# Kernel optimization log

Measured on AMD Instinct MI355X. Metric: run time of the kernel, lower is better.

The kernel has to match this reference:

```python
import jax, jax.numpy as jnp
import numpy as np

BETA_THRESH = 0.1   # threshold fraction in forward
BETA_IPOT = 0.5     # IPOT entropic beta
ITERATION = 30


def setup_inputs() -> dict:
    key = jax.random.key(0)
    k1, k2 = jax.random.split(key)
    bs, n, m, d = 64, 512, 512, 768
    return {
        "local_features_1": jax.random.normal(k1, (bs, n, d), dtype=jnp.float32),
        "local_features_2": jax.random.normal(k2, (bs, m, d), dtype=jnp.float32),
    }


def _wasserstein_loss(x, y):
    # x: (bs, n, d), y: (bs, m, d)
    # cost_matrix_batch_torch normalizes over the feature dim (dim=1 of bs*d*n layout)
    xn = x / (jnp.linalg.norm(x, axis=2, keepdims=True) + 1e-12)
    yn = y / (jnp.linalg.norm(y, axis=2, keepdims=True) + 1e-12)
    # cost_matrix returns (1 - cos).transpose(2,1); forward transposes back -> (bs, n, m)
    cos_distance = 1.0 - jnp.einsum("bnd,bmd->bnm", xn, yn)
    # global min/max threshold + relu
    min_score = cos_distance.min()
    max_score = cos_distance.max()
    threshold = min_score + BETA_THRESH * (max_score - min_score)
    C = jax.nn.relu(cos_distance - threshold)  # (bs, n, m)
    bs, n, m = C.shape
    A = jnp.exp(-C / BETA_IPOT)
    T0 = jnp.ones((bs, n, m), dtype=C.dtype)
    sigma0 = jnp.full((bs, m, 1), 1.0 / m, dtype=C.dtype)

    def step(carry, _):
        T, sigma = carry
        Q = A * T                                      # (bs, n, m)
        delta = 1.0 / (n * jnp.matmul(Q, sigma))       # (bs, n, 1)
        a = jnp.matmul(jnp.swapaxes(Q, 1, 2), delta)   # (bs, m, 1)
        sigma = 1.0 / (m * a)                          # (bs, m, 1)
        T = delta * Q * jnp.swapaxes(sigma, 1, 2)      # (bs, n, m)
        return (T, sigma), None

    (T, _), _ = jax.lax.scan(step, (T0, sigma0), None, length=ITERATION)
    # batch_trace(C^T @ T) == sum_ij C_ij * T_ij per batch element
    distance = jnp.einsum("bnm,bnm->b", C, T)
    # IPOT_distance returns -distance; loss is its mean
    return (-distance).mean()


def reference(local_features_1, local_features_2):
    return _wasserstein_loss(local_features_1, local_features_2)
```

## Files before the change

### kernel.cpp

```cpp
#include <hip/hip_runtime.h>
#include <hip/hip_fp16.h>

#define NN 512
#define DD 768

typedef _Float16 half8 __attribute__((ext_vector_type(8)));
typedef _Float16 half4 __attribute__((ext_vector_type(4)));
typedef _Float16 half2v __attribute__((ext_vector_type(2)));
typedef float f32x4 __attribute__((ext_vector_type(4)));

__device__ __forceinline__ int f2ord(float f) {
  int i = __float_as_int(f);
  return i < 0 ? (i ^ 0x7fffffff) : i;
}
__device__ __forceinline__ float ord2f(int i) {
  return __int_as_float(i < 0 ? (i ^ 0x7fffffff) : i);
}

__device__ __forceinline__ void glds16(const void* g, void* l) {
  __builtin_amdgcn_global_load_lds((const __attribute__((address_space(1))) void*)g,
                                   (__attribute__((address_space(3))) void*)l, 16, 0, 0);
}

__global__ __launch_bounds__(256) void k_norm(const float* __restrict__ f1,
                                              const float* __restrict__ f2,
                                              __half* __restrict__ xn,
                                              __half* __restrict__ yn,
                                              int* __restrict__ cnt) {
  if (blockIdx.x == 0) {
    int t = threadIdx.x;
    if (t < 64) { cnt[t * 16] = 0; cnt[1024 + t * 16] = 0; }
    if (t == 0) cnt[2048] = 0;
  }
  int row = blockIdx.x * 4 + (threadIdx.x >> 6);
  int lane = threadIdx.x & 63;
  int r = row & 32767;
  const float* src = (row < 32768 ? f1 : f2) + (size_t)r * DD;
  __half* dst = (row < 32768 ? xn : yn) + (size_t)r * DD;
  f32x4 v0 = *(const f32x4*)(src + lane * 4);
  f32x4 v1 = *(const f32x4*)(src + lane * 4 + 256);
  f32x4 v2 = *(const f32x4*)(src + lane * 4 + 512);
  float s = v0[0]*v0[0] + v0[1]*v0[1] + v0[2]*v0[2] + v0[3]*v0[3]
          + v1[0]*v1[0] + v1[1]*v1[1] + v1[2]*v1[2] + v1[3]*v1[3]
          + v2[0]*v2[0] + v2[1]*v2[1] + v2[2]*v2[2] + v2[3]*v2[3];
  #pragma unroll
  for (int m = 1; m < 64; m <<= 1) s += __shfl_xor(s, m, 64);
  float f = 1.0f / (sqrtf(s) + 1e-12f);
  union U { __half2 h2[2]; uint2 u; };
  U u0, u1, u2;
  u0.h2[0] = __floats2half2_rn(v0[0]*f, v0[1]*f); u0.h2[1] = __floats2half2_rn(v0[2]*f, v0[3]*f);
  u1.h2[0] = __floats2half2_rn(v1[0]*f, v1[1]*f); u1.h2[1] = __floats2half2_rn(v1[2]*f, v1[3]*f);
  u2.h2[0] = __floats2half2_rn(v2[0]*f, v2[1]*f); u2.h2[1] = __floats2half2_rn(v2[2]*f, v2[3]*f);
  *(uint2*)(dst + lane * 4)       = u0.u;
  *(uint2*)(dst + lane * 4 + 256) = u1.u;
  *(uint2*)(dst + lane * 4 + 512) = u2.u;
}

#define FOR16(X) X(0) X(1) X(2) X(3) X(4) X(5) X(6) X(7) X(8) X(9) X(10) X(11) X(12) X(13) X(14) X(15)

#define AGLD(p) __hip_atomic_load((p), __ATOMIC_RELAXED, __HIP_MEMORY_SCOPE_AGENT)
#define AGST(p, v) __hip_atomic_store((p), (v), __ATOMIC_RELAXED, __HIP_MEMORY_SCOPE_AGENT)
#define AGADD(p) __hip_atomic_fetch_add((p), 1, __ATOMIC_RELAXED, __HIP_MEMORY_SCOPE_AGENT)

struct IpotLds {
  float xs[128];
  float ys[NN];
  _Float16 zs[NN];
  _Float16 csh[8][520];
  float wred[8];
};
union MainLds {
  _Float16 Bs[2][16384];
  _Float16 At[4][8192];
  float mm[16];
  int mmi[16];
  IpotLds ip;
};

__global__ __launch_bounds__(512, 2) void k_main(const __half* __restrict__ xn,
                                                 const __half* __restrict__ yn,
                                                 int* __restrict__ cnt,
                                                 int* __restrict__ gmm,
                                                 unsigned* __restrict__ gpart,
                                                 float* __restrict__ gdist,
                                                 float* __restrict__ out) {
  __shared__ __align__(16) MainLds u;
  const int blk = blockIdx.x;
  const int b = blk & 63, qq = blk >> 6;
  const int tid = threadIdx.x;
  const int sv = tid >> 6, lane = tid & 63;
  const int fr = lane & 15;
  const int r0 = sv * 16;
  const int c0 = lane * 8;
  const int kg = lane >> 4;
  const int g8 = kg * 8;
  const int rslot = (kg ^ ((fr >> 1) & 3)) * 8;
  const __half* xnb = xn + ((size_t)b * NN + qq * 128 + sv * 16) * DD;
  const __half* ynb = yn + (size_t)b * NN * DD;

  f32x4 acc[32] = {};
  const int srcq = ((lane & 3) ^ ((lane >> 3) & 3)) * 8;
#define STAGE(bf, kk) { \
    _Pragma("unroll") \
    for (int j = 0; j < 4; ++j) { \
      const __half* ys_ = ynb + (size_t)(128 * j + sv * 16 + (lane >> 2)) * DD + (kk) + srcq; \
      glds16(ys_, (char*)u.Bs[bf] + j * 8192 + sv * 1024); \
    } }
  int buf = 0;
  STAGE(0, 0)
  half8 afp = *(const half8*)(xnb + (size_t)fr * DD + g8);
  for (int kk = 0; kk < DD; kk += 32) {
    __syncthreads();
    if (kk + 32 < DD) STAGE(buf ^ 1, kk + 32)
    half8 afc = afp;
    if (kk + 32 < DD) afp = *(const half8*)(xnb + (size_t)fr * DD + (kk + 32) + g8);
    #pragma unroll
    for (int c = 0; c < 32; ++c) {
      half8 bf = *(const half8*)(&u.Bs[buf][(16 * c + fr) * 32 + rslot]);
      acc[c] = __builtin_amdgcn_mfma_f32_16x16x32_f16(afc, bf, acc[c], 0, 0, 0);
    }
    buf ^= 1;
  }

  float vmin = 1e30f, vmax = -1e30f;
  #pragma unroll
  for (int c = 0; c < 32; ++c) {
    #pragma unroll
    for (int r2 = 0; r2 < 4; ++r2) {
      float val = 1.0f - acc[c][r2];
      vmin = fminf(vmin, val); vmax = fmaxf(vmax, val);
    }
  }
  #pragma unroll
  for (int m = 1; m < 64; m <<= 1) {
    vmin = fminf(vmin, __shfl_xor(vmin, m, 64));
    vmax = fmaxf(vmax, __shfl_xor(vmax, m, 64));
  }
  __syncthreads();
  if (lane == 0) { u.mm[sv] = vmin; u.mm[8 + sv] = vmax; }
  __syncthreads();
  if (tid == 0) {
    float bm = u.mm[0], bx = u.mm[8];
    #pragma unroll
    for (int g = 1; g < 8; ++g) { bm = fminf(bm, u.mm[g]); bx = fmaxf(bx, u.mm[8 + g]); }
    AGST(gmm + blk, (unsigned)f2ord(bm));
    AGST(gmm + 256 + blk, (unsigned)f2ord(bx));
  }
  __syncthreads();
  if (tid == 0) {
    int* c1p = cnt + 1024 + b * 16;
    AGADD(c1p);
    while (__hip_atomic_load(c1p, __ATOMIC_RELAXED, __HIP_MEMORY_SCOPE_AGENT) < 4)
      __builtin_amdgcn_s_sleep(1);
    if (qq == 0) AGADD(cnt + 2048);
    while (__hip_atomic_load(cnt + 2048, __ATOMIC_RELAXED, __HIP_MEMORY_SCOPE_AGENT) < 64)
      __builtin_amdgcn_s_sleep(8);
  }
  __syncthreads();
  {
    int mo = (int)AGLD(gmm + tid);
    #pragma unroll
    for (int m = 1; m < 64; m <<= 1) {
      int o = __shfl_xor(mo, m, 64);
      mo = (sv < 4) ? (mo < o ? mo : o) : (mo > o ? mo : o);
    }
    if (lane == 0) u.mmi[sv] = mo;
  }
  __syncthreads();
  int gmnord = u.mmi[0], gmxord = u.mmi[4];
  #pragma unroll
  for (int g = 1; g < 4; ++g) {
    gmnord = gmnord < u.mmi[g] ? gmnord : u.mmi[g];
    gmxord = gmxord > u.mmi[4 + g] ? gmxord : u.mmi[4 + g];
  }
  const float gmn = ord2f(gmnord);
  const float gmx = ord2f(gmxord);
  const float thr = gmn + 0.1f * (gmx - gmn);

#define DECLAM(r) half8 A##r, M##r;
  FOR16(DECLAM)

#define TWRITE { \
    _Float16* reg_ = u.At[sv & 3]; \
    const int q_ = lane >> 4; \
    _Pragma("unroll") \
    for (int c = 0; c < 32; ++c) { \
      _Pragma("unroll") \
      for (int r2 = 0; r2 < 4; ++r2) { \
        float val_ = 1.0f - acc[c][r2]; \
        float a_ = __expf(-2.0f * fmaxf(val_ - thr, 0.0f)); \
        int off_ = (((4 * q_ + r2) * 1024 + (16 * c + fr) * 2) ^ (q_ << 4)) >> 1; \
        reg_[off_] = (_Float16)a_; \
      } \
    } }

#define TREAD(r) { \
    A##r = *(const half8*)((const char*)u.At[sv & 3] + \
            (((r) * 1024 + lane * 16) ^ ((((r) >> 2) & 3) << 4))); \
    M##r = A##r; }

  __syncthreads();
  if (sv < 4) TWRITE
  __syncthreads();
  if (sv < 4) { FOR16(TREAD) }
  __syncthreads();
  if (sv >= 4) TWRITE
  __syncthreads();
  if (sv >= 4) { FOR16(TREAD) }
  __syncthreads();

  if (tid < 256) *(half2v*)(u.ip.zs + 2 * tid) = (half2v){(_Float16)1.0f, (_Float16)1.0f};
  u.ip.ys[tid] = 1.0f;
  __syncthreads();

  int* mycnt = cnt + b * 16;

  #pragma unroll 1
  for (int t = 1; t <= 30; ++t) {
    half8 zv = *(const half8*)(u.ip.zs + c0);
    float rp16[16];
#define ROWP(r) { \
      half8 p = M##r * zv; \
      half4 q = p.lo + p.hi; \
      half2v q2 = q.lo + q.hi; \
      rp16[r] = (float)q2.x + (float)q2.y; }
    FOR16(ROWP)
    float c8[8];
    #pragma unroll
    for (int i = 0; i < 8; ++i) {
      float keep = (lane & 1) ? rp16[2*i+1] : rp16[2*i];
      float send = (lane & 1) ? rp16[2*i]   : rp16[2*i+1];
      c8[i] = keep + __shfl_xor(send, 1, 64);
    }
    float c4[4];
    #pragma unroll
    for (int i = 0; i < 4; ++i) {
      float keep = (lane & 2) ? c8[2*i+1] : c8[2*i];
      float send = (lane & 2) ? c8[2*i]   : c8[2*i+1];
      c4[i] = keep + __shfl_xor(send, 2, 64);
    }
    float d2[2];
    #pragma unroll
    for (int i = 0; i < 2; ++i) {
      float keep = (lane & 4) ? c4[2*i+1] : c4[2*i];
      float send = (lane & 4) ? c4[2*i]   : c4[2*i+1];
      d2[i] = keep + __shfl_xor(send, 4, 64);
    }
    float c1;
    {
      float keep = (lane & 8) ? d2[1] : d2[0];
      float send = (lane & 8) ? d2[0] : d2[1];
      c1 = keep + __shfl_xor(send, 8, 64);
    }
    c1 += __shfl_xor(c1, 16, 64);
    c1 += __shfl_xor(c1, 32, 64);
    if (lane < 16) u.ip.xs[r0 + lane] = 1.0f / c1;
    half8 cac = (half8)(_Float16)0.0f;
#define COLP(r) { _Float16 xh = (_Float16)u.ip.xs[r0 + r]; cac += M##r * xh; }
    FOR16(COLP)
    *(half8*)(&u.ip.csh[sv][c0]) = cac;
    __syncthreads();
    unsigned* gp = gpart + ((size_t)((t & 1) * 256 + blk) * 256);
    if (tid < 256) {
      float a0 = 0.0f, a1 = 0.0f;
      #pragma unroll
      for (int g = 0; g < 8; ++g) {
        half2v pv = *(const half2v*)(&u.ip.csh[g][2 * tid]);
        a0 += (float)pv.x; a1 += (float)pv.y;
      }
      __half2 ph = __floats2half2_rn(a0, a1);
      AGST(gp + tid, *reinterpret_cast<unsigned*>(&ph));
    }
#define UPDM(r) M##r *= A##r;
    if (t < 30) { FOR16(UPDM) }
    __syncthreads();
    if (tid == 0) {
      AGADD(mycnt);
      while (__hip_atomic_load(mycnt, __ATOMIC_RELAXED, __HIP_MEMORY_SCOPE_AGENT) < 4 * t)
        __builtin_amdgcn_s_sleep(1);
    }
    __syncthreads();
    if (tid < 256) {
      float a0 = 0.0f, a1 = 0.0f;
      #pragma unroll
      for (int q2 = 0; q2 < 4; ++q2) {
        unsigned v = AGLD(gpart + ((size_t)((t & 1) * 256 + b + 64 * q2) * 256) + tid);
        __half2 h = *reinterpret_cast<__half2*>(&v);
        float2 fv = __half22float2(h);
        a0 += fv.x; a1 += fv.y;
      }
      float yo0 = u.ip.ys[2 * tid], yo1 = u.ip.ys[2 * tid + 1];
      float y0 = 1.0f / a0;
      float y1 = 1.0f / a1;
      *(half2v*)(u.ip.zs + 2 * tid) = (half2v){(_Float16)(y0 * y0 / yo0), (_Float16)(y1 * y1 / yo1)};
      u.ip.ys[2 * tid] = y0; u.ip.ys[2 * tid + 1] = y1;
    }
    __syncthreads();
  }

  float contrib = 0.0f;
#define FINP(r) { \
    float rowacc = 0.0f; \
    rowacc += -0.34657359f * __log2f((float)A##r.s0) * (float)M##r.s0 * u.ip.ys[c0 + 0]; \
    rowacc += -0.34657359f * __log2f((float)A##r.s1) * (float)M##r.s1 * u.ip.ys[c0 + 1]; \
    rowacc += -0.34657359f * __log2f((float)A##r.s2) * (float)M##r.s2 * u.ip.ys[c0 + 2]; \
    rowacc += -0.34657359f * __log2f((float)A##r.s3) * (float)M##r.s3 * u.ip.ys[c0 + 3]; \
    rowacc += -0.34657359f * __log2f((float)A##r.s4) * (float)M##r.s4 * u.ip.ys[c0 + 4]; \
    rowacc += -0.34657359f * __log2f((float)A##r.s5) * (float)M##r.s5 * u.ip.ys[c0 + 5]; \
    rowacc += -0.34657359f * __log2f((float)A##r.s6) * (float)M##r.s6 * u.ip.ys[c0 + 6]; \
    rowacc += -0.34657359f * __log2f((float)A##r.s7) * (float)M##r.s7 * u.ip.ys[c0 + 7]; \
    contrib += rowacc * u.ip.xs[r0 + r]; }
  FOR16(FINP)
  #pragma unroll
  for (int m = 1; m < 64; m <<= 1) contrib += __shfl_xor(contrib, m, 64);
  if (lane == 0) u.ip.wred[sv] = contrib;
  __syncthreads();
  if (tid == 0) {
    float s2 = 0.0f;
    #pragma unroll
    for (int g = 0; g < 8; ++g) s2 += u.ip.wred[g];
    AGST(gdist + blk, s2);
  }
  __syncthreads();
  if (tid == 0) AGADD(cnt + 2048);
  if (blk == 0) {
    if (tid == 0) {
      while (__hip_atomic_load(cnt + 2048, __ATOMIC_RELAXED, __HIP_MEMORY_SCOPE_AGENT) < 320)
        __builtin_amdgcn_s_sleep(8);
    }
    __syncthreads();
    if (tid < 64) {
      float v = AGLD(gdist + tid) + AGLD(gdist + tid + 64)
              + AGLD(gdist + tid + 128) + AGLD(gdist + tid + 192);
      #pragma unroll
      for (int m = 1; m < 64; m <<= 1) v += __shfl_xor(v, m, 64);
      if (tid == 0) out[0] = -v * (1.0f / (64.0f * 512.0f));
    }
  }
}

extern "C" void kernel_launch(void* const* d_in, const int* in_sizes, int n_in,
                              void* d_out, int out_size, void* d_ws, size_t ws_size,
                              hipStream_t stream) {
  const float* f1 = (const float*)d_in[0];
  const float* f2 = (const float*)d_in[1];
  char* ws = (char*)d_ws;
  __half* xn   = (__half*)(ws + 0);
  __half* yn   = (__half*)(ws + 50331648);
  unsigned* gpart = (unsigned*)(ws + 100663296);
  int*   cnt   = (int*)(ws + 167772160);
  int*   gmm   = (int*)(ws + 167772160 + 16384);
  float* gdist = (float*)(ws + 167772160 + 16384 + 2048);

  k_norm<<<16384, 256, 0, stream>>>(f1, f2, xn, yn, cnt);
  k_main<<<256, 512, 0, stream>>>(xn, yn, cnt, (int*)gmm, gpart, gdist, (float*)d_out);
}
```

Baseline: 191.2 us.

## Split each batch across eight 256-thread blocks instead of four 512-thread blocks

Reorganizes k_main so each batch element is handled by eight blocks of 256 threads (64 rows each) rather than four blocks of 512 threads (128 rows each), giving 512 blocks in total. The B-tile staging loop, the min/max reduction, the partial-column exchange buffers and the spin-barrier counts are all rescaled to match. The aim is to drop the serialized two-phase TWRITE/TREAD of the A tile and to spread work over more CUs. The cost is that every block now re-streams the full Y matrix for its batch, doubling Y traffic, and each IPOT barrier must wait on eight blocks, which means more cross-block synchronization and more partial reads per iteration. The spin barriers also assume all 512 blocks are co-resident, which at two blocks per CU depends on the device having at least 256 CUs.

```diff
diff --git a/kernel.cpp b/kernel.cpp
--- a/kernel.cpp
+++ b/kernel.cpp
@@ -63,11 +63,11 @@
 #define AGADD(p) __hip_atomic_fetch_add((p), 1, __ATOMIC_RELAXED, __HIP_MEMORY_SCOPE_AGENT)
 
 struct IpotLds {
-  float xs[128];
+  float xs[64];
   float ys[NN];
   _Float16 zs[NN];
-  _Float16 csh[8][520];
-  float wred[8];
+  _Float16 csh[4][520];
+  float wred[4];
 };
 union MainLds {
   _Float16 Bs[2][16384];
@@ -77,7 +77,7 @@
   IpotLds ip;
 };
 
-__global__ __launch_bounds__(512, 2) void k_main(const __half* __restrict__ xn,
+__global__ __launch_bounds__(256, 2) void k_main(const __half* __restrict__ xn,
                                                  const __half* __restrict__ yn,
                                                  int* __restrict__ cnt,
                                                  int* __restrict__ gmm,
@@ -86,7 +86,7 @@
                                                  float* __restrict__ out) {
   __shared__ __align__(16) MainLds u;
   const int blk = blockIdx.x;
-  const int b = blk & 63, qq = blk >> 6;
+  const int b = blk >> 3, qq = blk & 7;
   const int tid = threadIdx.x;
   const int sv = tid >> 6, lane = tid & 63;
   const int fr = lane & 15;
@@ -95,16 +95,16 @@
   const int kg = lane >> 4;
   const int g8 = kg * 8;
   const int rslot = (kg ^ ((fr >> 1) & 3)) * 8;
-  const __half* xnb = xn + ((size_t)b * NN + qq * 128 + sv * 16) * DD;
+  const __half* xnb = xn + ((size_t)b * NN + qq * 64 + sv * 16) * DD;
   const __half* ynb = yn + (size_t)b * NN * DD;
 
   f32x4 acc[32] = {};
   const int srcq = ((lane & 3) ^ ((lane >> 3) & 3)) * 8;
 #define STAGE(bf, kk) { \
     _Pragma("unroll") \
-    for (int j = 0; j < 4; ++j) { \
-      const __half* ys_ = ynb + (size_t)(128 * j + sv * 16 + (lane >> 2)) * DD + (kk) + srcq; \
-      glds16(ys_, (char*)u.Bs[bf] + j * 8192 + sv * 1024); \
+    for (int j = 0; j < 8; ++j) { \
+      const __half* ys_ = ynb + (size_t)(64 * j + sv * 16 + (lane >> 2)) * DD + (kk) + srcq; \
+      glds16(ys_, (char*)u.Bs[bf] + j * 4096 + sv * 1024); \
     } }
   int buf = 0;
   STAGE(0, 0)
@@ -142,15 +142,15 @@
   if (tid == 0) {
     float bm = u.mm[0], bx = u.mm[8];
     #pragma unroll
-    for (int g = 1; g < 8; ++g) { bm = fminf(bm, u.mm[g]); bx = fmaxf(bx, u.mm[8 + g]); }
-    AGST(gmm + blk, (unsigned)f2ord(bm));
-    AGST(gmm + 256 + blk, (unsigned)f2ord(bx));
+    for (int g = 1; g < 4; ++g) { bm = fminf(bm, u.mm[g]); bx = fmaxf(bx, u.mm[8 + g]); }
+    AGST(gmm + blk, f2ord(bm));
+    AGST(gmm + 512 + blk, f2ord(bx));
   }
   __syncthreads();
   if (tid == 0) {
     int* c1p = cnt + 1024 + b * 16;
     AGADD(c1p);
-    while (__hip_atomic_load(c1p, __ATOMIC_RELAXED, __HIP_MEMORY_SCOPE_AGENT) < 4)
+    while (__hip_atomic_load(c1p, __ATOMIC_RELAXED, __HIP_MEMORY_SCOPE_AGENT) < 8)
       __builtin_amdgcn_s_sleep(1);
     if (qq == 0) AGADD(cnt + 2048);
     while (__hip_atomic_load(cnt + 2048, __ATOMIC_RELAXED, __HIP_MEMORY_SCOPE_AGENT) < 64)
@@ -158,20 +158,23 @@
   }
   __syncthreads();
   {
-    int mo = (int)AGLD(gmm + tid);
+    int mn0 = AGLD(gmm + tid), mn1 = AGLD(gmm + 256 + tid);
+    int mx0 = AGLD(gmm + 512 + tid), mx1 = AGLD(gmm + 768 + tid);
+    int mn = mn0 < mn1 ? mn0 : mn1;
+    int mx = mx0 > mx1 ? mx0 : mx1;
     #pragma unroll
     for (int m = 1; m < 64; m <<= 1) {
-      int o = __shfl_xor(mo, m, 64);
-      mo = (sv < 4) ? (mo < o ? mo : o) : (mo > o ? mo : o);
-    }
-    if (lane == 0) u.mmi[sv] = mo;
-  }
-  __syncthreads();
-  int gmnord = u.mmi[0], gmxord = u.mmi[4];
+      int o = __shfl_xor(mn, m, 64); mn = mn < o ? mn : o;
+      o = __shfl_xor(mx, m, 64);     mx = mx > o ? mx : o;
+    }
+    if (lane == 0) { u.mmi[sv] = mn; u.mmi[8 + sv] = mx; }
+  }
+  __syncthreads();
+  int gmnord = u.mmi[0], gmxord = u.mmi[8];
   #pragma unroll
   for (int g = 1; g < 4; ++g) {
     gmnord = gmnord < u.mmi[g] ? gmnord : u.mmi[g];
-    gmxord = gmxord > u.mmi[4 + g] ? gmxord : u.mmi[4 + g];
+    gmxord = gmxord > u.mmi[8 + g] ? gmxord : u.mmi[8 + g];
   }
   const float gmn = ord2f(gmnord);
   const float gmx = ord2f(gmxord);
@@ -181,7 +184,7 @@
   FOR16(DECLAM)
 
 #define TWRITE { \
-    _Float16* reg_ = u.At[sv & 3]; \
+    _Float16* reg_ = u.At[sv]; \
     const int q_ = lane >> 4; \
     _Pragma("unroll") \
     for (int c = 0; c < 32; ++c) { \
@@ -195,22 +198,19 @@
     } }
 
 #define TREAD(r) { \
-    A##r = *(const half8*)((const char*)u.At[sv & 3] + \
+    A##r = *(const half8*)((const char*)u.At[sv] + \
             (((r) * 1024 + lane * 16) ^ ((((r) >> 2) & 3) << 4))); \
     M##r = A##r; }
 
   __syncthreads();
-  if (sv < 4) TWRITE
-  __syncthreads();
-  if (sv < 4) { FOR16(TREAD) }
-  __syncthreads();
-  if (sv >= 4) TWRITE
-  __syncthreads();
-  if (sv >= 4) { FOR16(TREAD) }
-  __syncthreads();
-
-  if (tid < 256) *(half2v*)(u.ip.zs + 2 * tid) = (half2v){(_Float16)1.0f, (_Float16)1.0f};
+  TWRITE
+  __syncthreads();
+  FOR16(TREAD)
+  __syncthreads();
+
+  *(half2v*)(u.ip.zs + 2 * tid) = (half2v){(_Float16)1.0f, (_Float16)1.0f};
   u.ip.ys[tid] = 1.0f;
+  u.ip.ys[tid + 256] = 1.0f;
   __syncthreads();
 
   int* mycnt = cnt + b * 16;
@@ -260,11 +260,11 @@
     FOR16(COLP)
     *(half8*)(&u.ip.csh[sv][c0]) = cac;
     __syncthreads();
-    unsigned* gp = gpart + ((size_t)((t & 1) * 256 + blk) * 256);
-    if (tid < 256) {
+    unsigned* gp = gpart + ((size_t)((t & 1) * 512 + blk) * 256);
+    {
       float a0 = 0.0f, a1 = 0.0f;
       #pragma unroll
-      for (int g = 0; g < 8; ++g) {
+      for (int g = 0; g < 4; ++g) {
         half2v pv = *(const half2v*)(&u.ip.csh[g][2 * tid]);
         a0 += (float)pv.x; a1 += (float)pv.y;
       }
@@ -276,15 +276,16 @@
     __syncthreads();
     if (tid == 0) {
       AGADD(mycnt);
-      while (__hip_atomic_load(mycnt, __ATOMIC_RELAXED, __HIP_MEMORY_SCOPE_AGENT) < 4 * t)
+      while (__hip_atomic_load(mycnt, __ATOMIC_RELAXED, __HIP_MEMORY_SCOPE_AGENT) < 8 * t)
         __builtin_amdgcn_s_sleep(1);
     }
     __syncthreads();
-    if (tid < 256) {
+    {
       float a0 = 0.0f, a1 = 0.0f;
+      const unsigned* pbase = gpart + ((size_t)((t & 1) * 512 + 8 * b) * 256) + tid;
       #pragma unroll
-      for (int q2 = 0; q2 < 4; ++q2) {
-        unsigned v = AGLD(gpart + ((size_t)((t & 1) * 256 + b + 64 * q2) * 256) + tid);
+      for (int q2 = 0; q2 < 8; ++q2) {
+        unsigned v = AGLD(pbase + q2 * 256);
         __half2 h = *reinterpret_cast<__half2*>(&v);
         float2 fv = __half22float2(h);
         a0 += fv.x; a1 += fv.y;
@@ -318,20 +319,21 @@
   if (tid == 0) {
     float s2 = 0.0f;
     #pragma unroll
-    for (int g = 0; g < 8; ++g) s2 += u.ip.wred[g];
+    for (int g = 0; g < 4; ++g) s2 += u.ip.wred[g];
     AGST(gdist + blk, s2);
   }
   __syncthreads();
   if (tid == 0) AGADD(cnt + 2048);
   if (blk == 0) {
     if (tid == 0) {
-      while (__hip_atomic_load(cnt + 2048, __ATOMIC_RELAXED, __HIP_MEMORY_SCOPE_AGENT) < 320)
+      while (__hip_atomic_load(cnt + 2048, __ATOMIC_RELAXED, __HIP_MEMORY_SCOPE_AGENT) < 576)
         __builtin_amdgcn_s_sleep(8);
     }
     __syncthreads();
     if (tid < 64) {
-      float v = AGLD(gdist + tid) + AGLD(gdist + tid + 64)
-              + AGLD(gdist + tid + 128) + AGLD(gdist + tid + 192);
+      float v = 0.0f;
+      #pragma unroll
+      for (int q2 = 0; q2 < 8; ++q2) v += AGLD(gdist + 8 * tid + q2);
       #pragma unroll
       for (int m = 1; m < 64; m <<= 1) v += __shfl_xor(v, m, 64);
       if (tid == 0) out[0] = -v * (1.0f / (64.0f * 512.0f));
@@ -350,8 +352,8 @@
   unsigned* gpart = (unsigned*)(ws + 100663296);
   int*   cnt   = (int*)(ws + 167772160);
   int*   gmm   = (int*)(ws + 167772160 + 16384);
-  float* gdist = (float*)(ws + 167772160 + 16384 + 2048);
+  float* gdist = (float*)(ws + 167772160 + 16384 + 4096);
 
   k_norm<<<16384, 256, 0, stream>>>(f1, f2, xn, yn, cnt);
-  k_main<<<256, 512, 0, stream>>>(xn, yn, cnt, (int*)gmm, gpart, gdist, (float*)d_out);
-}
+  k_main<<<512, 256, 0, stream>>>(xn, yn, cnt, (int*)gmm, gpart, gdist, (float*)d_out);
+}
```

New measurement: 266.0 us. +39.1%, slower.
